# Optimization experiments

Measured on AMD Instinct MI355X. Metric: run time of the kernel, lower is better.

Reference implementation:

```python
import jax, jax.numpy as jnp
import numpy as np

IN_DIM = 2048
OUT_DIM = 1536
N_PARAM = max(IN_DIM, OUT_DIM)  # 2048


def setup_inputs() -> dict:
    key = jax.random.key(0)
    k1, k2, k3 = jax.random.split(key, 3)
    x = jax.random.normal(k1, (8, 64, 64, IN_DIM), dtype=jnp.float32)
    # NOTE: original init is zeros for W_first_col (output would be all-zero);
    # we use randn so the reference computes something non-trivial.
    W_first_col = jax.random.normal(k2, (N_PARAM,), dtype=jnp.float32)
    W_second_col = jax.random.normal(k3, (N_PARAM,), dtype=jnp.float32)
    return {"x": x, "W_first_col": W_first_col, "W_second_col": W_second_col}


def reference(x, W_first_col, W_second_col):
    # Effective first column of the circulant matrix, truncated to in_dim
    W = (W_first_col * W_second_col)[:IN_DIM]            # [C]
    W_fft = jnp.fft.fft(W)                               # [C] complex64
    x_fft = jnp.fft.fft(x, axis=-1)                      # [B,H,W,C] complex64
    result = jnp.fft.ifft(W_fft * x_fft, axis=-1).real   # circular conv along channels
    return result[..., :OUT_DIM]                         # [B,H,W,out_dim]
```

## Files before the change

kernel.cpp:

```cpp
#include <hip/hip_runtime.h>
#include <math.h>

#define C_LEN 2048
#define HALF  1024
#define OUTD  1536
#define NPIX  32768
#define LDSW  1088

#define FENCE() __builtin_amdgcn_sched_barrier(0)

__device__ __forceinline__ int SWZ(int idx) { return idx ^ ((idx >> 5) & 31); }

template<int DIR>
__device__ void fft2048(float* r0, float* i0, float* r1, float* i1, int t) {
    float *sr = r0, *si = i0, *dr = r1, *di = i1;
    const float TW = (float)DIR * 6.283185307179586f / 2048.0f;
    const float FD = (float)DIR;
    __syncthreads();
    #pragma unroll
    for (int b = 0; b < 4; ++b) {
        int t2 = t + b * 256;
        float ar = sr[SWZ(t2)],        ai = si[SWZ(t2)];
        float br = sr[SWZ(t2 + 1024)], bi = si[SWZ(t2 + 1024)];
        float sn, cs;
        sincosf(TW * (float)t2, &sn, &cs);
        float vr = ar - br, vi = ai - bi;
        int w0 = 2 * t2;
        dr[SWZ(w0)]     = ar + br;
        di[SWZ(w0)]     = ai + bi;
        dr[SWZ(w0 + 1)] = cs * vr - sn * vi;
        di[SWZ(w0 + 1)] = cs * vi + sn * vr;
    }
    { float* tp; tp = sr; sr = dr; dr = tp; tp = si; si = di; di = tp; }
    #pragma unroll
    for (int m = 2; m <= 512; m *= 4) {
        __syncthreads();
        #pragma unroll
        for (int b = 0; b < 2; ++b) {
            int t2 = t + b * 256;
            int jm = t2 & ~(m - 1);
            float a0r = sr[SWZ(t2)],        a0i = si[SWZ(t2)];
            float a1r = sr[SWZ(t2 + 512)],  a1i = si[SWZ(t2 + 512)];
            float a2r = sr[SWZ(t2 + 1024)], a2i = si[SWZ(t2 + 1024)];
            float a3r = sr[SWZ(t2 + 1536)], a3i = si[SWZ(t2 + 1536)];
            float s0r = a0r + a2r, s0i = a0i + a2i;
            float d0r = a0r - a2r, d0i = a0i - a2i;
            float s1r = a1r + a3r, s1i = a1i + a3i;
            float d1r = a1r - a3r, d1i = a1i - a3i;
            float A0r = s0r + s1r, A0i = s0i + s1i;
            float A2r = s0r - s1r, A2i = s0i - s1i;
            float A1r = d0r - FD * d1i, A1i = d0i + FD * d1r;
            float A3r = d0r + FD * d1i, A3i = d0i - FD * d1r;
            float s1w, c1w;
            sincosf(TW * (float)jm, &s1w, &c1w);
            float c2w = c1w * c1w - s1w * s1w, s2w = 2.0f * c1w * s1w;
            float c3w = c1w * c2w - s1w * s2w, s3w = c1w * s2w + s1w * c2w;
            int wb = t2 + 3 * jm;
            dr[SWZ(wb)]         = A0r;
            di[SWZ(wb)]         = A0i;
            dr[SWZ(wb + m)]     = c1w * A1r - s1w * A1i;
            di[SWZ(wb + m)]     = c1w * A1i + s1w * A1r;
            dr[SWZ(wb + 2 * m)] = c2w * A2r - s2w * A2i;
            di[SWZ(wb + 2 * m)] = c2w * A2i + s2w * A2r;
            dr[SWZ(wb + 3 * m)] = c3w * A3r - s3w * A3i;
            di[SWZ(wb + 3 * m)] = c3w * A3i + s3w * A3r;
        }
        { float* tp; tp = sr; sr = dr; dr = tp; tp = si; si = di; di = tp; }
    }
    __syncthreads();
}

__global__ __launch_bounds__(256)
void uv_kernel(const float* __restrict__ w1, const float* __restrict__ w2,
               float4* __restrict__ uv) {
    __shared__ float r0[C_LEN], i0[C_LEN], r1[C_LEN], i1[C_LEN];
    int t = threadIdx.x;
    #pragma unroll
    for (int k = 0; k < 8; ++k) {
        int e = t + k * 256;
        r0[SWZ(e)] = w1[e] * w2[e];
        i0[SWZ(e)] = 0.0f;
    }
    fft2048<-1>(r0, i0, r1, i1, t);
    #pragma unroll
    for (int b = 0; b < 4; ++b) {
        int k = t + b * 256;
        float w1r = r0[SWZ(k)],        w1i = i0[SWZ(k)];
        float w2r = r0[SWZ(k + 1024)], w2i = i0[SWZ(k + 1024)];
        float Sr = (w1r + w2r) * (1.0f / 4096.0f);
        float Si = (w1i + w2i) * (1.0f / 4096.0f);
        float Dr = (w1r - w2r) * (1.0f / 4096.0f);
        float Di = (w1i - w2i) * (1.0f / 4096.0f);
        float sn, cs;
        sincosf((6.283185307179586f / 2048.0f) * (float)k, &sn, &cs);
        float Er = cs * Dr - sn * Di, Ei = cs * Di + sn * Dr;
        float Fr = cs * Dr + sn * Di, Fi = cs * Di - sn * Dr;
        uv[k] = make_float4(Sr - Ei, Si + Er, Sr + Fi, Si - Fr);
    }
}

__device__ __forceinline__ void cm(float& or_, float& oi_, float ar, float ai,
                                   float br, float bi) {
    or_ = ar * br - ai * bi;
    oi_ = ar * bi + ai * br;
}

template<int S>
__device__ __forceinline__ void fft16_ip(float* xr, float* xi) {
    const float FS = (float)S;
    const float C1 = 0.9238795325112867f;
    const float S1 = 0.3826834323650898f;
    const float R2 = 0.7071067811865476f;
    #pragma unroll
    for (int n0 = 0; n0 < 4; ++n0) {
        float a0r = xr[n0],      a0i = xi[n0];
        float a1r = xr[n0 + 4],  a1i = xi[n0 + 4];
        float a2r = xr[n0 + 8],  a2i = xi[n0 + 8];
        float a3r = xr[n0 + 12], a3i = xi[n0 + 12];
        float t0r = a0r + a2r, t0i = a0i + a2i;
        float t1r = a0r - a2r, t1i = a0i - a2i;
        float t2r = a1r + a3r, t2i = a1i + a3i;
        float t3r = a1r - a3r, t3i = a1i - a3i;
        float y1r = t1r - FS * t3i, y1i = t1i + FS * t3r;
        float y2r = t0r - t2r,      y2i = t0i - t2i;
        float y3r = t1r + FS * t3i, y3i = t1i - FS * t3r;
        xr[n0] = t0r + t2r;  xi[n0] = t0i + t2i;
        if (n0 == 0) {
            xr[4]  = y1r; xi[4]  = y1i;
            xr[8]  = y2r; xi[8]  = y2i;
            xr[12] = y3r; xi[12] = y3i;
        } else if (n0 == 1) {
            cm(xr[5],  xi[5],  y1r, y1i, C1,  FS * S1);
            cm(xr[9],  xi[9],  y2r, y2i, R2,  FS * R2);
            cm(xr[13], xi[13], y3r, y3i, S1,  FS * C1);
        } else if (n0 == 2) {
            cm(xr[6],  xi[6],  y1r, y1i, R2,  FS * R2);
            xr[10] = -FS * y2i;  xi[10] = FS * y2r;
            cm(xr[14], xi[14], y3r, y3i, -R2, FS * R2);
        } else {
            cm(xr[7],  xi[7],  y1r, y1i, S1,  FS * C1);
            cm(xr[11], xi[11], y2r, y2i, -R2, FS * R2);
            cm(xr[15], xi[15], y3r, y3i, -C1, -FS * S1);
        }
    }
    #pragma unroll
    for (int k0 = 0; k0 < 4; ++k0) {
        float b0r = xr[4 * k0],     b0i = xi[4 * k0];
        float b1r = xr[4 * k0 + 1], b1i = xi[4 * k0 + 1];
        float b2r = xr[4 * k0 + 2], b2i = xi[4 * k0 + 2];
        float b3r = xr[4 * k0 + 3], b3i = xi[4 * k0 + 3];
        float t0r = b0r + b2r, t0i = b0i + b2i;
        float t1r = b0r - b2r, t1i = b0i - b2i;
        float t2r = b1r + b3r, t2i = b1i + b3i;
        float t3r = b1r - b3r, t3i = b1i - b3i;
        xr[4 * k0]     = t0r + t2r;      xi[4 * k0]     = t0i + t2i;
        xr[4 * k0 + 1] = t1r - FS * t3i; xi[4 * k0 + 1] = t1i + FS * t3r;
        xr[4 * k0 + 2] = t0r - t2r;      xi[4 * k0 + 2] = t0i - t2i;
        xr[4 * k0 + 3] = t1r + FS * t3i; xi[4 * k0 + 3] = t1i - FS * t3r;
    }
}

__device__ __forceinline__ void tw_store2(const float* vrA, const float* viA,
                                          const float* vrB, const float* viB,
                                          float4* row, int xorv, float th) {
    float bs, bc;
    __sincosf(th, &bs, &bc);
    float aR[4], aI[4], bR[4], bI[4];
    aR[0] = 1.f; aI[0] = 0.f;
    aR[1] = bc;  aI[1] = bs;
    aR[2] = bc * bc - bs * bs;          aI[2] = 2.f * bc * bs;
    aR[3] = aR[2] * bc - aI[2] * bs;    aI[3] = aR[2] * bs + aI[2] * bc;
    bR[0] = 1.f; bI[0] = 0.f;
    bR[1] = aR[2] * aR[2] - aI[2] * aI[2];  bI[1] = 2.f * aR[2] * aI[2];
    bR[2] = bR[1] * bR[1] - bI[1] * bI[1];  bI[2] = 2.f * bR[1] * bI[1];
    bR[3] = bR[2] * bR[1] - bI[2] * bI[1];  bI[3] = bR[2] * bI[1] + bI[2] * bR[1];
    #pragma unroll
    for (int c = 0; c < 16; ++c) {
        int p = ((c & 3) << 2) | (c >> 2);
        float wr = aR[c & 3] * bR[c >> 2] - aI[c & 3] * bI[c >> 2];
        float wi = aR[c & 3] * bI[c >> 2] + aI[c & 3] * bR[c >> 2];
        float xA = vrA[p] * wr - viA[p] * wi;
        float yA = vrA[p] * wi + viA[p] * wr;
        float xB = vrB[p] * wr - viB[p] * wi;
        float yB = vrB[p] * wi + viB[p] * wr;
        row[c ^ xorv] = make_float4(xA, yA, xB, yB);
    }
}

__global__ __launch_bounds__(64, 2)
void conv64x2(const float* __restrict__ x, const float4* __restrict__ uv,
              float2* __restrict__ out) {
    __shared__ float4 lds[LDSW];
    const int t = threadIdx.x;
    const size_t pixA = (size_t)blockIdx.x << 1;
    const float2* xpA = reinterpret_cast<const float2*>(x) + pixA * (size_t)HALF;
    const float2* xpB = xpA + HALF;

    float vrA[16], viA[16], vrB[16], viB[16];
    #pragma unroll
    for (int a = 0; a < 16; ++a) {
        float2 zA = xpA[(a << 6) + t];
        float2 zB = xpB[(a << 6) + t];
        vrA[a] = zA.x; viA[a] = zA.y;
        vrB[a] = zB.x; viB[a] = zB.y;
    }

    fft16_ip<-1>(vrA, viA);
    fft16_ip<-1>(vrB, viB);
    tw_store2(vrA, viA, vrB, viB, lds + t * 17, 0,
              (-6.283185307179586f / 1024.0f) * (float)t);
    FENCE();
    {
        const int f = t & 3, c = t >> 2;
        const float4* rp = lds + f * 17 + c;
        #pragma unroll
        for (int e = 0; e < 16; ++e) {
            float4 z = rp[e * 68];
            vrA[e] = z.x; viA[e] = z.y; vrB[e] = z.z; viB[e] = z.w;
        }
        FENCE();
        fft16_ip<-1>(vrA, viA);
        fft16_ip<-1>(vrB, viB);
        tw_store2(vrA, viA, vrB, viB, lds + (t << 4), c,
                  (-6.283185307179586f / 64.0f) * (float)f);
    }
    FENCE();
    {
        const int q = t & 3, c = t >> 2;
        float drA[16], diA[16], drB[16], diB[16];
        #pragma unroll
        for (int f2 = 0; f2 < 4; ++f2) {
            #pragma unroll
            for (int s = 0; s < 4; ++s) {
                int wrow = (c << 2) + f2;
                float4 z = lds[(wrow << 4) + (((q << 2) + s) ^ c)];
                drA[f2 * 4 + s] = z.x; diA[f2 * 4 + s] = z.y;
                drB[f2 * 4 + s] = z.z; diB[f2 * 4 + s] = z.w;
            }
        }
        FENCE();
        #pragma unroll
        for (int s = 0; s < 4; ++s) {
            int kb = c + (q << 6) + (s << 4);
            {
                float ar = drA[0 + s],  ai = diA[0 + s];
                float br = drA[4 + s],  bi = diA[4 + s];
                float cr = drA[8 + s],  ci = diA[8 + s];
                float er = drA[12 + s], ei = diA[12 + s];
                float t0r = ar + cr, t0i = ai + ci;
                float t1r = ar - cr, t1i = ai - ci;
                float t2r = br + er, t2i = bi + ei;
                float t3r = br - er, t3i = bi - ei;
                float Br = drB[0 + s],  Bi = diB[0 + s];
                float Cr = drB[4 + s],  Ci = diB[4 + s];
                float Dr = drB[8 + s],  Di = diB[8 + s];
                float Er = drB[12 + s], Ei = diB[12 + s];
                float u0r = Br + Dr, u0i = Bi + Di;
                float u1r = Br - Dr, u1i = Bi - Di;
                float u2r = Cr + Er, u2i = Ci + Ei;
                float u3r = Cr - Er, u3i = Ci - Ei;
                lds[kb]       = make_float4(t0r + t2r, t0i + t2i,
                                            u0r + u2r, u0i + u2i);
                lds[kb + 256] = make_float4(t1r + t3i, t1i - t3r,
                                            u1r + u3i, u1i - u3r);
                lds[kb + 512] = make_float4(t0r - t2r, t0i - t2i,
                                            u0r - u2r, u0i - u2i);
                lds[kb + 768] = make_float4(t1r - t3i, t1i + t3r,
                                            u1r - u3i, u1i + u3r);
            }
        }
    }
    FENCE();

    #pragma unroll
    for (int a = 0; a < 16; ++a) {
        int k = (a << 6) + t;
        float4 Za = lds[k];
        float4 Zm = lds[(HALF - k) & (HALF - 1)];
        float4 u  = uv[k];
        {
            float Ar = Za.x + Zm.x, Ai = Za.y - Zm.y;
            float Br = Za.x - Zm.x, Bi = Za.y + Zm.y;
            vrA[a] = Ar * u.x - Ai * u.y + Br * u.z - Bi * u.w;
            viA[a] = Ar * u.y + Ai * u.x + Br * u.w + Bi * u.z;
        }
        {
            float Ar = Za.z + Zm.z, Ai = Za.w - Zm.w;
            float Br = Za.z - Zm.z, Bi = Za.w + Zm.w;
            vrB[a] = Ar * u.x - Ai * u.y + Br * u.z - Bi * u.w;
            viB[a] = Ar * u.y + Ai * u.x + Br * u.w + Bi * u.z;
        }
    }
    FENCE();

    fft16_ip<1>(vrA, viA);
    fft16_ip<1>(vrB, viB);
    tw_store2(vrA, viA, vrB, viB, lds + t * 17, 0,
              (6.283185307179586f / 1024.0f) * (float)t);
    FENCE();
    {
        const int f = t & 3, c = t >> 2;
        const float4* rp = lds + f * 17 + c;
        #pragma unroll
        for (int e = 0; e < 16; ++e) {
            float4 z = rp[e * 68];
            vrA[e] = z.x; viA[e] = z.y; vrB[e] = z.z; viB[e] = z.w;
        }
        FENCE();
        fft16_ip<1>(vrA, viA);
        fft16_ip<1>(vrB, viB);
        tw_store2(vrA, viA, vrB, viB, lds + (t << 4), c,
                  (6.283185307179586f / 64.0f) * (float)f);
    }
    FENCE();
    {
        const int q = t & 3, c = t >> 2;
        float drA[16], diA[16], drB[16], diB[16];
        #pragma unroll
        for (int f2 = 0; f2 < 4; ++f2) {
            #pragma unroll
            for (int s = 0; s < 4; ++s) {
                int wrow = (c << 2) + f2;
                float4 z = lds[(wrow << 4) + (((q << 2) + s) ^ c)];
                drA[f2 * 4 + s] = z.x; diA[f2 * 4 + s] = z.y;
                drB[f2 * 4 + s] = z.z; diB[f2 * 4 + s] = z.w;
            }
        }
        float2* opA = out + pixA * (size_t)(OUTD / 2);
        float2* opB = opA + (OUTD / 2);
        #pragma unroll
        for (int s = 0; s < 4; ++s) {
            int nb = c + (q << 6) + (s << 4);
            {
                float ar = drA[0 + s],  ai = diA[0 + s];
                float br = drA[4 + s],  bi = diA[4 + s];
                float cr = drA[8 + s],  ci = diA[8 + s];
                float er = drA[12 + s], ei = diA[12 + s];
                float t0r = ar + cr, t0i = ai + ci;
                float t1r = ar - cr, t1i = ai - ci;
                float t2r = br + er, t2i = bi + ei;
                float t3r = br - er, t3i = bi - ei;
                opA[nb]       = make_float2(t0r + t2r, t0i + t2i);
                opA[nb + 256] = make_float2(t1r - t3i, t1i + t3r);
                opA[nb + 512] = make_float2(t0r - t2r, t0i - t2i);
            }
            {
                float ar = drB[0 + s],  ai = diB[0 + s];
                float br = drB[4 + s],  bi = diB[4 + s];
                float cr = drB[8 + s],  ci = diB[8 + s];
                float er = drB[12 + s], ei = diB[12 + s];
                float t0r = ar + cr, t0i = ai + ci;
                float t1r = ar - cr, t1i = ai - ci;
                float t2r = br + er, t2i = bi + ei;
                float t3r = br - er, t3i = bi - ei;
                opB[nb]       = make_float2(t0r + t2r, t0i + t2i);
                opB[nb + 256] = make_float2(t1r - t3i, t1i + t3r);
                opB[nb + 512] = make_float2(t0r - t2r, t0i - t2i);
            }
        }
    }
}

extern "C" void kernel_launch(void* const* d_in, const int* in_sizes, int n_in,
                              void* d_out, int out_size, void* d_ws, size_t ws_size,
                              hipStream_t stream) {
    const float* x  = (const float*)d_in[0];
    const float* w1 = (const float*)d_in[1];
    const float* w2 = (const float*)d_in[2];
    float2* out = (float2*)d_out;
    float4* uv  = (float4*)d_ws;

    hipLaunchKernelGGL(uv_kernel, dim3(1), dim3(256), 0, stream, w1, w2, uv);
    hipLaunchKernelGGL(conv64x2, dim3(NPIX / 2), dim3(64), 0, stream, x, uv, out);
}
```

Baseline: 128.6 us.

## Software-pipeline two pixels through half-size float2 LDS, two waves per block

Measured after the change: 352.0 us. 174% more time.

```diff
diff --git a/kernel.cpp b/kernel.cpp
--- a/kernel.cpp
+++ b/kernel.cpp
@@ -160,41 +160,50 @@
     }
 }
 
-__device__ __forceinline__ void tw_store2(const float* vrA, const float* viA,
-                                          const float* vrB, const float* viB,
-                                          float4* row, int xorv, float th) {
+struct Tw { float aR[4], aI[4], bR[4], bI[4]; };
+
+__device__ __forceinline__ void tw_make(float th, Tw& w) {
     float bs, bc;
     __sincosf(th, &bs, &bc);
-    float aR[4], aI[4], bR[4], bI[4];
-    aR[0] = 1.f; aI[0] = 0.f;
-    aR[1] = bc;  aI[1] = bs;
-    aR[2] = bc * bc - bs * bs;          aI[2] = 2.f * bc * bs;
-    aR[3] = aR[2] * bc - aI[2] * bs;    aI[3] = aR[2] * bs + aI[2] * bc;
-    bR[0] = 1.f; bI[0] = 0.f;
-    bR[1] = aR[2] * aR[2] - aI[2] * aI[2];  bI[1] = 2.f * aR[2] * aI[2];
-    bR[2] = bR[1] * bR[1] - bI[1] * bI[1];  bI[2] = 2.f * bR[1] * bI[1];
-    bR[3] = bR[2] * bR[1] - bI[2] * bI[1];  bI[3] = bR[2] * bI[1] + bI[2] * bR[1];
+    w.aR[0] = 1.f; w.aI[0] = 0.f;
+    w.aR[1] = bc;  w.aI[1] = bs;
+    w.aR[2] = bc * bc - bs * bs;             w.aI[2] = 2.f * bc * bs;
+    w.aR[3] = w.aR[2] * bc - w.aI[2] * bs;   w.aI[3] = w.aR[2] * bs + w.aI[2] * bc;
+    w.bR[0] = 1.f; w.bI[0] = 0.f;
+    w.bR[1] = w.aR[2] * w.aR[2] - w.aI[2] * w.aI[2];  w.bI[1] = 2.f * w.aR[2] * w.aI[2];
+    w.bR[2] = w.bR[1] * w.bR[1] - w.bI[1] * w.bI[1];  w.bI[2] = 2.f * w.bR[1] * w.bI[1];
+    w.bR[3] = w.bR[2] * w.bR[1] - w.bI[2] * w.bI[1];  w.bI[3] = w.bR[2] * w.bI[1] + w.bI[2] * w.bR[1];
+}
+
+template<int CONJ>
+__device__ __forceinline__ void tw_apply_store(const float* vr, const float* vi,
+                                               float2* row, int xorv, const Tw& w) {
     #pragma unroll
     for (int c = 0; c < 16; ++c) {
         int p = ((c & 3) << 2) | (c >> 2);
-        float wr = aR[c & 3] * bR[c >> 2] - aI[c & 3] * bI[c >> 2];
-        float wi = aR[c & 3] * bI[c >> 2] + aI[c & 3] * bR[c >> 2];
-        float xA = vrA[p] * wr - viA[p] * wi;
-        float yA = vrA[p] * wi + viA[p] * wr;
-        float xB = vrB[p] * wr - viB[p] * wi;
-        float yB = vrB[p] * wi + viB[p] * wr;
-        row[c ^ xorv] = make_float4(xA, yA, xB, yB);
-    }
-}
-
-__global__ __launch_bounds__(64, 2)
-void conv64x2(const float* __restrict__ x, const float4* __restrict__ uv,
+        float wr = w.aR[c & 3] * w.bR[c >> 2] - w.aI[c & 3] * w.bI[c >> 2];
+        float wi = w.aR[c & 3] * w.bI[c >> 2] + w.aI[c & 3] * w.bR[c >> 2];
+        if (CONJ) wi = -wi;
+        float x = vr[p] * wr - vi[p] * wi;
+        float y = vr[p] * wi + vi[p] * wr;
+        row[c ^ xorv] = make_float2(x, y);
+    }
+}
+
+__global__ __launch_bounds__(128, 4)
+void conv2pix(const float* __restrict__ x, const float4* __restrict__ uv,
               float2* __restrict__ out) {
-    __shared__ float4 lds[LDSW];
-    const int t = threadIdx.x;
-    const size_t pixA = (size_t)blockIdx.x << 1;
+    __shared__ float2 ldsAll[2 * LDSW];
+    const int tid = threadIdx.x;
+    const int t   = tid & 63;
+    const int wid = tid >> 6;
+    float2* lds = ldsAll + wid * LDSW;
+    const size_t pixA = ((size_t)blockIdx.x << 2) + ((size_t)wid << 1);
     const float2* xpA = reinterpret_cast<const float2*>(x) + pixA * (size_t)HALF;
     const float2* xpB = xpA + HALF;
+
+    const int f = t & 3, c = t >> 2;
+    const int q = t & 3;
 
     float vrA[16], viA[16], vrB[16], viB[16];
     #pragma unroll
@@ -207,157 +216,204 @@
 
     fft16_ip<-1>(vrA, viA);
     fft16_ip<-1>(vrB, viB);
-    tw_store2(vrA, viA, vrB, viB, lds + t * 17, 0,
-              (-6.283185307179586f / 1024.0f) * (float)t);
-    FENCE();
-    {
-        const int f = t & 3, c = t >> 2;
-        const float4* rp = lds + f * 17 + c;
+    FENCE();
+    Tw w1;
+    tw_make((-6.283185307179586f / 1024.0f) * (float)t, w1);
+    tw_apply_store<0>(vrA, viA, lds + t * 17, 0, w1);
+    FENCE();
+    {
+        const float2* rp = lds + f * 17 + c;
         #pragma unroll
         for (int e = 0; e < 16; ++e) {
-            float4 z = rp[e * 68];
-            vrA[e] = z.x; viA[e] = z.y; vrB[e] = z.z; viB[e] = z.w;
-        }
-        FENCE();
-        fft16_ip<-1>(vrA, viA);
-        fft16_ip<-1>(vrB, viB);
-        tw_store2(vrA, viA, vrB, viB, lds + (t << 4), c,
-                  (-6.283185307179586f / 64.0f) * (float)f);
-    }
-    FENCE();
-    {
-        const int q = t & 3, c = t >> 2;
-        float drA[16], diA[16], drB[16], diB[16];
+            float2 z = rp[e * 68];
+            vrA[e] = z.x; viA[e] = z.y;
+        }
+        tw_apply_store<0>(vrB, viB, lds + t * 17, 0, w1);
+    }
+    FENCE();
+    fft16_ip<-1>(vrA, viA);
+    {
+        const float2* rp = lds + f * 17 + c;
+        #pragma unroll
+        for (int e = 0; e < 16; ++e) {
+            float2 z = rp[e * 68];
+            vrB[e] = z.x; viB[e] = z.y;
+        }
+    }
+    FENCE();
+    Tw w2;
+    tw_make((-6.283185307179586f / 64.0f) * (float)f, w2);
+    tw_apply_store<0>(vrA, viA, lds + (t << 4), c, w2);
+    fft16_ip<-1>(vrB, viB);
+    FENCE();
+    {
         #pragma unroll
         for (int f2 = 0; f2 < 4; ++f2) {
             #pragma unroll
             for (int s = 0; s < 4; ++s) {
                 int wrow = (c << 2) + f2;
-                float4 z = lds[(wrow << 4) + (((q << 2) + s) ^ c)];
-                drA[f2 * 4 + s] = z.x; diA[f2 * 4 + s] = z.y;
-                drB[f2 * 4 + s] = z.z; diB[f2 * 4 + s] = z.w;
+                float2 z = lds[(wrow << 4) + (((q << 2) + s) ^ c)];
+                vrA[f2 * 4 + s] = z.x; viA[f2 * 4 + s] = z.y;
             }
         }
-        FENCE();
-        #pragma unroll
-        for (int s = 0; s < 4; ++s) {
-            int kb = c + (q << 6) + (s << 4);
-            {
-                float ar = drA[0 + s],  ai = diA[0 + s];
-                float br = drA[4 + s],  bi = diA[4 + s];
-                float cr = drA[8 + s],  ci = diA[8 + s];
-                float er = drA[12 + s], ei = diA[12 + s];
-                float t0r = ar + cr, t0i = ai + ci;
-                float t1r = ar - cr, t1i = ai - ci;
-                float t2r = br + er, t2i = bi + ei;
-                float t3r = br - er, t3i = bi - ei;
-                float Br = drB[0 + s],  Bi = diB[0 + s];
-                float Cr = drB[4 + s],  Ci = diB[4 + s];
-                float Dr = drB[8 + s],  Di = diB[8 + s];
-                float Er = drB[12 + s], Ei = diB[12 + s];
-                float u0r = Br + Dr, u0i = Bi + Di;
-                float u1r = Br - Dr, u1i = Bi - Di;
-                float u2r = Cr + Er, u2i = Ci + Ei;
-                float u3r = Cr - Er, u3i = Ci - Ei;
-                lds[kb]       = make_float4(t0r + t2r, t0i + t2i,
-                                            u0r + u2r, u0i + u2i);
-                lds[kb + 256] = make_float4(t1r + t3i, t1i - t3r,
-                                            u1r + u3i, u1i - u3r);
-                lds[kb + 512] = make_float4(t0r - t2r, t0i - t2i,
-                                            u0r - u2r, u0i - u2i);
-                lds[kb + 768] = make_float4(t1r - t3i, t1i + t3r,
-                                            u1r - u3i, u1i + u3r);
-            }
-        }
-    }
-    FENCE();
-
-    #pragma unroll
-    for (int a = 0; a < 16; ++a) {
-        int k = (a << 6) + t;
-        float4 Za = lds[k];
-        float4 Zm = lds[(HALF - k) & (HALF - 1)];
-        float4 u  = uv[k];
-        {
-            float Ar = Za.x + Zm.x, Ai = Za.y - Zm.y;
-            float Br = Za.x - Zm.x, Bi = Za.y + Zm.y;
-            vrA[a] = Ar * u.x - Ai * u.y + Br * u.z - Bi * u.w;
-            viA[a] = Ar * u.y + Ai * u.x + Br * u.w + Bi * u.z;
-        }
-        {
-            float Ar = Za.z + Zm.z, Ai = Za.w - Zm.w;
-            float Br = Za.z - Zm.z, Bi = Za.w + Zm.w;
-            vrB[a] = Ar * u.x - Ai * u.y + Br * u.z - Bi * u.w;
-            viB[a] = Ar * u.y + Ai * u.x + Br * u.w + Bi * u.z;
-        }
-    }
-    FENCE();
-
-    fft16_ip<1>(vrA, viA);
-    fft16_ip<1>(vrB, viB);
-    tw_store2(vrA, viA, vrB, viB, lds + t * 17, 0,
-              (6.283185307179586f / 1024.0f) * (float)t);
-    FENCE();
-    {
-        const int f = t & 3, c = t >> 2;
-        const float4* rp = lds + f * 17 + c;
-        #pragma unroll
-        for (int e = 0; e < 16; ++e) {
-            float4 z = rp[e * 68];
-            vrA[e] = z.x; viA[e] = z.y; vrB[e] = z.z; viB[e] = z.w;
-        }
-        FENCE();
-        fft16_ip<1>(vrA, viA);
-        fft16_ip<1>(vrB, viB);
-        tw_store2(vrA, viA, vrB, viB, lds + (t << 4), c,
-                  (6.283185307179586f / 64.0f) * (float)f);
-    }
-    FENCE();
-    {
-        const int q = t & 3, c = t >> 2;
-        float drA[16], diA[16], drB[16], diB[16];
+        tw_apply_store<0>(vrB, viB, lds + (t << 4), c, w2);
+    }
+    FENCE();
+    {
         #pragma unroll
         for (int f2 = 0; f2 < 4; ++f2) {
             #pragma unroll
             for (int s = 0; s < 4; ++s) {
                 int wrow = (c << 2) + f2;
-                float4 z = lds[(wrow << 4) + (((q << 2) + s) ^ c)];
-                drA[f2 * 4 + s] = z.x; diA[f2 * 4 + s] = z.y;
-                drB[f2 * 4 + s] = z.z; diB[f2 * 4 + s] = z.w;
+                float2 z = lds[(wrow << 4) + (((q << 2) + s) ^ c)];
+                vrB[f2 * 4 + s] = z.x; viB[f2 * 4 + s] = z.y;
             }
         }
-        float2* opA = out + pixA * (size_t)(OUTD / 2);
-        float2* opB = opA + (OUTD / 2);
-        #pragma unroll
-        for (int s = 0; s < 4; ++s) {
-            int nb = c + (q << 6) + (s << 4);
-            {
-                float ar = drA[0 + s],  ai = diA[0 + s];
-                float br = drA[4 + s],  bi = diA[4 + s];
-                float cr = drA[8 + s],  ci = diA[8 + s];
-                float er = drA[12 + s], ei = diA[12 + s];
-                float t0r = ar + cr, t0i = ai + ci;
-                float t1r = ar - cr, t1i = ai - ci;
-                float t2r = br + er, t2i = bi + ei;
-                float t3r = br - er, t3i = bi - ei;
-                opA[nb]       = make_float2(t0r + t2r, t0i + t2i);
-                opA[nb + 256] = make_float2(t1r - t3i, t1i + t3r);
-                opA[nb + 512] = make_float2(t0r - t2r, t0i - t2i);
+    }
+    FENCE();
+    #pragma unroll
+    for (int s = 0; s < 4; ++s) {
+        float ar = vrA[0 + s],  ai = viA[0 + s];
+        float br = vrA[4 + s],  bi = viA[4 + s];
+        float cr = vrA[8 + s],  ci = viA[8 + s];
+        float er = vrA[12 + s], ei = viA[12 + s];
+        float t0r = ar + cr, t0i = ai + ci;
+        float t1r = ar - cr, t1i = ai - ci;
+        float t2r = br + er, t2i = bi + ei;
+        float t3r = br - er, t3i = bi - ei;
+        int kb = c + (q << 6) + (s << 4);
+        lds[kb]       = make_float2(t0r + t2r, t0i + t2i);
+        lds[kb + 256] = make_float2(t1r + t3i, t1i - t3r);
+        lds[kb + 512] = make_float2(t0r - t2r, t0i - t2i);
+        lds[kb + 768] = make_float2(t1r - t3i, t1i + t3r);
+    }
+    FENCE();
+    #pragma unroll
+    for (int a = 0; a < 16; ++a) {
+        int k = (a << 6) + t;
+        float2 Za = lds[k];
+        float2 Zm = lds[(HALF - k) & (HALF - 1)];
+        float4 u  = uv[k];
+        float Ar = Za.x + Zm.x, Ai = Za.y - Zm.y;
+        float Br = Za.x - Zm.x, Bi = Za.y + Zm.y;
+        vrA[a] = Ar * u.x - Ai * u.y + Br * u.z - Bi * u.w;
+        viA[a] = Ar * u.y + Ai * u.x + Br * u.w + Bi * u.z;
+    }
+    FENCE();
+    #pragma unroll
+    for (int s = 0; s < 4; ++s) {
+        float ar = vrB[0 + s],  ai = viB[0 + s];
+        float br = vrB[4 + s],  bi = viB[4 + s];
+        float cr = vrB[8 + s],  ci = viB[8 + s];
+        float er = vrB[12 + s], ei = viB[12 + s];
+        float t0r = ar + cr, t0i = ai + ci;
+        float t1r = ar - cr, t1i = ai - ci;
+        float t2r = br + er, t2i = bi + ei;
+        float t3r = br - er, t3i = bi - ei;
+        int kb = c + (q << 6) + (s << 4);
+        lds[kb]       = make_float2(t0r + t2r, t0i + t2i);
+        lds[kb + 256] = make_float2(t1r + t3i, t1i - t3r);
+        lds[kb + 512] = make_float2(t0r - t2r, t0i - t2i);
+        lds[kb + 768] = make_float2(t1r - t3i, t1i + t3r);
+    }
+    fft16_ip<1>(vrA, viA);
+    FENCE();
+    #pragma unroll
+    for (int a = 0; a < 16; ++a) {
+        int k = (a << 6) + t;
+        float2 Za = lds[k];
+        float2 Zm = lds[(HALF - k) & (HALF - 1)];
+        float4 u  = uv[k];
+        float Ar = Za.x + Zm.x, Ai = Za.y - Zm.y;
+        float Br = Za.x - Zm.x, Bi = Za.y + Zm.y;
+        vrB[a] = Ar * u.x - Ai * u.y + Br * u.z - Bi * u.w;
+        viB[a] = Ar * u.y + Ai * u.x + Br * u.w + Bi * u.z;
+    }
+    FENCE();
+
+    tw_make((-6.283185307179586f / 1024.0f) * (float)t, w1);
+    tw_apply_store<1>(vrA, viA, lds + t * 17, 0, w1);
+    fft16_ip<1>(vrB, viB);
+    FENCE();
+    {
+        const float2* rp = lds + f * 17 + c;
+        #pragma unroll
+        for (int e = 0; e < 16; ++e) {
+            float2 z = rp[e * 68];
+            vrA[e] = z.x; viA[e] = z.y;
+        }
+        tw_apply_store<1>(vrB, viB, lds + t * 17, 0, w1);
+    }
+    FENCE();
+    fft16_ip<1>(vrA, viA);
+    {
+        const float2* rp = lds + f * 17 + c;
+        #pragma unroll
+        for (int e = 0; e < 16; ++e) {
+            float2 z = rp[e * 68];
+            vrB[e] = z.x; viB[e] = z.y;
+        }
+    }
+    FENCE();
+    tw_make((-6.283185307179586f / 64.0f) * (float)f, w2);
+    tw_apply_store<1>(vrA, viA, lds + (t << 4), c, w2);
+    fft16_ip<1>(vrB, viB);
+    FENCE();
+    {
+        #pragma unroll
+        for (int f2 = 0; f2 < 4; ++f2) {
+            #pragma unroll
+            for (int s = 0; s < 4; ++s) {
+                int wrow = (c << 2) + f2;
+                float2 z = lds[(wrow << 4) + (((q << 2) + s) ^ c)];
+                vrA[f2 * 4 + s] = z.x; viA[f2 * 4 + s] = z.y;
             }
-            {
-                float ar = drB[0 + s],  ai = diB[0 + s];
-                float br = drB[4 + s],  bi = diB[4 + s];
-                float cr = drB[8 + s],  ci = diB[8 + s];
-                float er = drB[12 + s], ei = diB[12 + s];
-                float t0r = ar + cr, t0i = ai + ci;
-                float t1r = ar - cr, t1i = ai - ci;
-                float t2r = br + er, t2i = bi + ei;
-                float t3r = br - er, t3i = bi - ei;
-                opB[nb]       = make_float2(t0r + t2r, t0i + t2i);
-                opB[nb + 256] = make_float2(t1r - t3i, t1i + t3r);
-                opB[nb + 512] = make_float2(t0r - t2r, t0i - t2i);
+        }
+        tw_apply_store<1>(vrB, viB, lds + (t << 4), c, w2);
+    }
+    FENCE();
+    float2* opA = out + pixA * (size_t)(OUTD / 2);
+    float2* opB = opA + (OUTD / 2);
+    #pragma unroll
+    for (int s = 0; s < 4; ++s) {
+        float ar = vrA[0 + s],  ai = viA[0 + s];
+        float br = vrA[4 + s],  bi = viA[4 + s];
+        float cr = vrA[8 + s],  ci = viA[8 + s];
+        float er = vrA[12 + s], ei = viA[12 + s];
+        float t0r = ar + cr, t0i = ai + ci;
+        float t1r = ar - cr, t1i = ai - ci;
+        float t2r = br + er, t2i = bi + ei;
+        float t3r = br - er, t3i = bi - ei;
+        int nb = c + (q << 6) + (s << 4);
+        opA[nb]       = make_float2(t0r + t2r, t0i + t2i);
+        opA[nb + 256] = make_float2(t1r - t3i, t1i + t3r);
+        opA[nb + 512] = make_float2(t0r - t2r, t0i - t2i);
+    }
+    {
+        #pragma unroll
+        for (int f2 = 0; f2 < 4; ++f2) {
+            #pragma unroll
+            for (int s = 0; s < 4; ++s) {
+                int wrow = (c << 2) + f2;
+                float2 z = lds[(wrow << 4) + (((q << 2) + s) ^ c)];
+                vrB[f2 * 4 + s] = z.x; viB[f2 * 4 + s] = z.y;
             }
         }
+    }
+    #pragma unroll
+    for (int s = 0; s < 4; ++s) {
+        float ar = vrB[0 + s],  ai = viB[0 + s];
+        float br = vrB[4 + s],  bi = viB[4 + s];
+        float cr = vrB[8 + s],  ci = viB[8 + s];
+        float er = vrB[12 + s], ei = viB[12 + s];
+        float t0r = ar + cr, t0i = ai + ci;
+        float t1r = ar - cr, t1i = ai - ci;
+        float t2r = br + er, t2i = bi + ei;
+        float t3r = br - er, t3i = bi - ei;
+        int nb = c + (q << 6) + (s << 4);
+        opB[nb]       = make_float2(t0r + t2r, t0i + t2i);
+        opB[nb + 256] = make_float2(t1r - t3i, t1i + t3r);
+        opB[nb + 512] = make_float2(t0r - t2r, t0i - t2i);
     }
 }
 
@@ -371,5 +427,5 @@
     float4* uv  = (float4*)d_ws;
 
     hipLaunchKernelGGL(uv_kernel, dim3(1), dim3(256), 0, stream, w1, w2, uv);
-    hipLaunchKernelGGL(conv64x2, dim3(NPIX / 2), dim3(64), 0, stream, x, uv, out);
-}
+    hipLaunchKernelGGL(conv2pix, dim3(NPIX / 4), dim3(128), 0, stream, x, uv, out);
+}
```
